# Optimization experiments

Hardware: AMD Instinct MI355X
Metric: run time of the kernel (lower is better)

The kernel has to match this reference:

```python
import jax, jax.numpy as jnp
import numpy as np

N_NODES = 10000
N_EDGES = 320000
IN_DIM = 512
HID = 128


def setup_inputs() -> dict:
    key = jax.random.key(0)
    k1, k2, k3, k4 = jax.random.split(key, 4)
    x = jax.random.normal(k1, (N_NODES, IN_DIM), dtype=jnp.float32)
    edge_index = jax.random.randint(k2, (2, N_EDGES), 0, N_NODES, dtype=jnp.int64)
    W_enc = jax.random.normal(k3, (IN_DIM, HID), dtype=jnp.float32) * 0.05
    b_enc = jnp.zeros((HID,), dtype=jnp.float32)
    W_dec = jax.random.normal(k4, (HID, N_NODES), dtype=jnp.float32) * 0.05
    b_dec = jnp.zeros((N_NODES,), dtype=jnp.float32)
    return {"x": x, "edge_index": edge_index, "W_enc": W_enc, "b_enc": b_enc,
            "W_dec": W_dec, "b_dec": b_dec}


def reference(x, edge_index, W_enc, b_enc, W_dec, b_dec):
    N = x.shape[0]
    # ---- GCNConv (PyG defaults: self-loops + symmetric normalization) ----
    h = x @ W_enc                                  # [N, HID]
    loops = jnp.arange(N, dtype=edge_index.dtype)
    src = jnp.concatenate([edge_index[0], loops])  # source j
    dst = jnp.concatenate([edge_index[1], loops])  # target i
    ones = jnp.ones(src.shape[0], dtype=h.dtype)
    deg = jax.ops.segment_sum(ones, dst, num_segments=N)          # in-degree incl. self-loop
    dinv = jnp.where(deg > 0, jax.lax.rsqrt(deg), 0.0)
    norm = dinv[src] * dinv[dst]                                   # [E+N]
    msgs = h[src] * norm[:, None]                                  # gather-scale
    agg = jax.ops.segment_sum(msgs, dst, num_segments=N)           # scatter-add [N, HID]
    encoded = agg + b_enc
    # ---- decoder: Linear + sigmoid ----
    decoded = jax.nn.sigmoid(encoded @ W_dec + b_dec)              # [N, N]
    return decoded
```

## Files before the change

kernel.cpp:

```cpp
#include <hip/hip_runtime.h>
#include <hip/hip_bf16.h>

#define N_NODES 10000
#define IN_DIM 512
#define HID 128
#define NPAD 10240

typedef __attribute__((ext_vector_type(8))) __bf16 bf16x8;
typedef __attribute__((ext_vector_type(8))) unsigned short u16x8;
typedef __attribute__((ext_vector_type(4))) float f32x4;

__device__ __forceinline__ unsigned short f2bf(float f) {
    unsigned int u = __float_as_uint(f);
    return (unsigned short)((u + 0x7fffu + ((u >> 16) & 1u)) >> 16);
}

__device__ __forceinline__ void gload_lds16(const void* g, void* l) {
    __builtin_amdgcn_global_load_lds(
        (const __attribute__((address_space(1))) unsigned int*)g,
        (__attribute__((address_space(3))) unsigned int*)l, 16, 0, 0);
}

__global__ void k_prep(const float* __restrict__ w, __hip_bfloat16* __restrict__ wT,
                       int* __restrict__ cnt) {
    int b = blockIdx.x;
    if (b < 40) {
        cnt[b * 256 + threadIdx.x] = 0;
        return;
    }
    int idx = (b - 40) * 256 + threadIdx.x;
    int n = idx & (HID - 1);
    int k = idx >> 7;
    wT[n * IN_DIM + k] = __float2bfloat16(w[k * HID + n]);
}

__global__ void k_hist(const int* __restrict__ ei, int* cnt, int E) {
    int e = blockIdx.x * 256 + threadIdx.x;
    if (e < E) atomicAdd(&cnt[ei[E + e]], 1);
}

__global__ __launch_bounds__(1024) void k_scan(
    const int* __restrict__ cnt, int* __restrict__ base,
    int* __restrict__ cursor, float* __restrict__ dinv) {
    __shared__ int lds[1024];
    int t = threadIdx.x;
    int loc[10];
    int sum = 0;
#pragma unroll
    for (int j = 0; j < 10; ++j) {
        int idx = t * 10 + j;
        int c = cnt[idx];
        loc[j] = sum;
        sum += c;
    }
    lds[t] = sum;
    __syncthreads();
    for (int off = 1; off < 1024; off <<= 1) {
        int v = (t >= off) ? lds[t - off] : 0;
        __syncthreads();
        lds[t] += v;
        __syncthreads();
    }
    int ex = lds[t] - sum;
#pragma unroll
    for (int j = 0; j < 10; ++j) {
        int idx = t * 10 + j;
        int b = ex + loc[j];
        base[idx] = b;
        cursor[idx] = b;
        dinv[idx] = rsqrtf((float)cnt[idx] + 1.0f);
    }
}

__global__ void k_fill(const int* __restrict__ ei, const float* __restrict__ dinv,
                       int* cursor, int2* __restrict__ csr, int E) {
    int e = blockIdx.x * 256 + threadIdx.x;
    if (e >= E) return;
    int s = ei[e];
    int d = ei[E + e];
    int pos = atomicAdd(&cursor[d], 1);
    float w = dinv[s] * dinv[d];
    csr[pos] = make_int2(s, __float_as_int(w));
}

__global__ __launch_bounds__(256) void k_wdec_t(const float* __restrict__ wdec,
                                                __hip_bfloat16* __restrict__ wT) {
    __shared__ float tile[32][33];
    int tx = threadIdx.x, ty = threadIdx.y;
    int n0 = blockIdx.x * 32, k0 = blockIdx.y * 32;
#pragma unroll
    for (int j = 0; j < 4; ++j) {
        int k = k0 + ty * 4 + j;
        int n = n0 + tx;
        tile[ty * 4 + j][tx] = (n < N_NODES) ? wdec[(size_t)k * N_NODES + n] : 0.0f;
    }
    __syncthreads();
#pragma unroll
    for (int j = 0; j < 4; ++j) {
        int n = n0 + ty * 4 + j;
        int k = k0 + tx;
        wT[(size_t)n * HID + k] = __float2bfloat16(tile[tx][ty * 4 + j]);
    }
}

__global__ __launch_bounds__(256) void k_enc_gemm(
    const float* __restrict__ x, const __hip_bfloat16* __restrict__ wencT,
    float* __restrict__ h)
{
    int tid = threadIdx.x;
    int wv = tid >> 6, lane = tid & 63;
    int l16 = lane & 15, quad = lane >> 4;
    int m_w = blockIdx.x * 32 + (wv >> 1) * 16;
    int n_w = (wv & 1) * 64;
    f32x4 acc[4] = {};
    int row = m_w + l16;
    bool rv = row < N_NODES;
    const float* xr = x + (size_t)row * IN_DIM;
    for (int kk = 0; kk < IN_DIM; kk += 32) {
        int k0 = kk + quad * 8;
        f32x4 u = {}, w = {};
        if (rv) {
            u = *(const f32x4*)(xr + k0);
            w = *(const f32x4*)(xr + k0 + 4);
        }
        union { u16x8 u; bf16x8 v; } a;
#pragma unroll
        for (int j = 0; j < 4; ++j) {
            a.u[j] = f2bf(u[j]);
            a.u[4 + j] = f2bf(w[j]);
        }
        bf16x8 b[4];
#pragma unroll
        for (int ni = 0; ni < 4; ++ni)
            b[ni] = *(const bf16x8*)(const void*)(wencT + (size_t)(n_w + ni * 16 + l16) * IN_DIM + k0);
#pragma unroll
        for (int ni = 0; ni < 4; ++ni)
            acc[ni] = __builtin_amdgcn_mfma_f32_16x16x32_bf16(a.v, b[ni], acc[ni], 0, 0, 0);
    }
#pragma unroll
    for (int ni = 0; ni < 4; ++ni) {
        int n = n_w + ni * 16 + l16;
#pragma unroll
        for (int r = 0; r < 4; ++r) {
            int m = m_w + quad * 4 + r;
            if (m < N_NODES) h[(size_t)m * HID + n] = acc[ni][r];
        }
    }
}

__global__ __launch_bounds__(256) void k_agg_enc(
    const float* __restrict__ h, const int2* __restrict__ csr,
    const int* __restrict__ base, const int* __restrict__ cnt,
    const float* __restrict__ dinv, const float* __restrict__ b_enc,
    __hip_bfloat16* __restrict__ enc)
{
    int i = blockIdx.x * 2 + (threadIdx.x >> 7);
    int ch = threadIdx.x & 127;
    if (i >= N_NODES) {
        enc[(size_t)i * HID + ch] = __float2bfloat16(0.0f);
        return;
    }
    int lane = threadIdx.x & 63;
    float di = dinv[i];
    float a0 = di * di * h[(size_t)i * HID + ch];
    float a1 = 0.0f, a2 = 0.0f, a3 = 0.0f;
    int j0 = base[i], d = cnt[i];
    for (int b = 0; b < d; b += 64) {
        int cw = d - b;
        if (cw > 64) cw = 64;
        int2 p = make_int2(0, 0);
        if (lane < cw) p = csr[j0 + b + lane];
        int px = p.x, py = p.y;
        int j = 0;
        for (; j + 4 <= cw; j += 4) {
            int s0 = __shfl(px, j),     s1 = __shfl(px, j + 1);
            int s2 = __shfl(px, j + 2), s3 = __shfl(px, j + 3);
            float w0 = __int_as_float(__shfl(py, j));
            float w1 = __int_as_float(__shfl(py, j + 1));
            float w2 = __int_as_float(__shfl(py, j + 2));
            float w3 = __int_as_float(__shfl(py, j + 3));
            a0 += w0 * h[(size_t)s0 * HID + ch];
            a1 += w1 * h[(size_t)s1 * HID + ch];
            a2 += w2 * h[(size_t)s2 * HID + ch];
            a3 += w3 * h[(size_t)s3 * HID + ch];
        }
        for (; j < cw; ++j) {
            int s = __shfl(px, j);
            float w = __int_as_float(__shfl(py, j));
            a0 += w * h[(size_t)s * HID + ch];
        }
    }
    enc[(size_t)i * HID + ch] = __float2bfloat16(((a0 + a1) + (a2 + a3)) + b_enc[ch]);
}

__global__ __launch_bounds__(256) void k_dec_gemm(
    const __hip_bfloat16* __restrict__ A, const __hip_bfloat16* __restrict__ BT,
    const float* __restrict__ bias, float* __restrict__ C)
{
    extern __shared__ char lds[];
    char* ldsA = lds;
    char* ldsB = lds + 32768;

    const int NT = 80;
    int orig = blockIdx.x;
    int wg = (orig & 7) * 800 + (orig >> 3);
    int bx = wg % NT, by = wg / NT;

    int tid = threadIdx.x;
    int wv = tid >> 6, lane = tid & 63;
    int l16 = lane & 15, quad = lane >> 4;
    int wm = wv >> 1, wn = wv & 1;

    {
        const char* gA = (const char*)A + (size_t)by * 32768;
        const char* gB = (const char*)BT + (size_t)bx * 32768;
        int wb = wv * 1024;
#pragma unroll
        for (int it = 0; it < 8; ++it) {
            int L = wb + it * 4096 + lane * 16;
            int row = L >> 8;
            int src = (row << 8) | ((L & 255) ^ ((row & 7) << 4));
            gload_lds16(gA + src, ldsA + wb + it * 4096);
        }
#pragma unroll
        for (int it = 0; it < 8; ++it) {
            int L = wb + it * 4096 + lane * 16;
            int row = L >> 8;
            int src = (row << 8) | ((L & 255) ^ ((row & 7) << 4));
            gload_lds16(gB + src, ldsB + wb + it * 4096);
        }
    }
    asm volatile("s_waitcnt vmcnt(0)" ::: "memory");
    __syncthreads();

    f32x4 acc[4][4] = {};
    int qb = quad * 16;
#pragma unroll
    for (int ks = 0; ks < 4; ++ks) {
        int kb = ks * 64 + qb;
        bf16x8 a[4], b[4];
#pragma unroll
        for (int ni = 0; ni < 4; ++ni) {
            int r = wn * 64 + ni * 16 + l16;
            b[ni] = *(const bf16x8*)(ldsB + ((r << 8) + (kb ^ ((r & 7) << 4))));
        }
#pragma unroll
        for (int mi = 0; mi < 4; ++mi) {
            int r = wm * 64 + mi * 16 + l16;
            a[mi] = *(const bf16x8*)(ldsA + ((r << 8) + (kb ^ ((r & 7) << 4))));
        }
#pragma unroll
        for (int mi = 0; mi < 4; ++mi)
#pragma unroll
            for (int ni = 0; ni < 4; ++ni)
                acc[mi][ni] = __builtin_amdgcn_mfma_f32_16x16x32_bf16(b[ni], a[mi], acc[mi][ni], 0, 0, 0);
    }

    int m_w = by * 128 + wm * 64;
    int n_w = bx * 128 + wn * 64;
    f32x4 bv[4];
#pragma unroll
    for (int ni = 0; ni < 4; ++ni) {
        int n4 = n_w + ni * 16 + quad * 4;
        bv[ni] = (n4 < N_NODES) ? *(const f32x4*)(bias + n4) : f32x4{};
    }
#pragma unroll
    for (int mi = 0; mi < 4; ++mi) {
        int m = m_w + mi * 16 + l16;
        if (m >= N_NODES) continue;
        size_t rowoff = (size_t)m * N_NODES;
#pragma unroll
        for (int ni = 0; ni < 4; ++ni) {
            int n4 = n_w + ni * 16 + quad * 4;
            if (n4 >= N_NODES) continue;
            f32x4 z = acc[mi][ni];
            f32x4 s;
#pragma unroll
            for (int r = 0; r < 4; ++r) {
                float e = __expf(-(z[r] + bv[ni][r]));
                s[r] = __builtin_amdgcn_rcpf(1.0f + e);
            }
            *(f32x4*)(C + rowoff + n4) = s;
        }
    }
}

extern "C" void kernel_launch(void* const* d_in, const int* in_sizes, int n_in,
                              void* d_out, int out_size, void* d_ws, size_t ws_size,
                              hipStream_t stream) {
    const float* x     = (const float*)d_in[0];
    const int*   ei    = (const int*)d_in[1];
    const float* W_enc = (const float*)d_in[2];
    const float* b_enc = (const float*)d_in[3];
    const float* W_dec = (const float*)d_in[4];
    const float* b_dec = (const float*)d_in[5];
    float* out = (float*)d_out;
    const int E = in_sizes[1] / 2;

    char* p = (char*)d_ws;
    auto carve = [&](size_t bytes) -> char* {
        char* r = p;
        p += (bytes + 255) & ~(size_t)255;
        return r;
    };
    int*   cnt    = (int*)carve((size_t)NPAD * 4);
    int*   base   = (int*)carve((size_t)NPAD * 4);
    int*   cursor = (int*)carve((size_t)NPAD * 4);
    float* dinv   = (float*)carve((size_t)NPAD * 4);
    int2*  csr    = (int2*)carve((size_t)E * 8);
    float* h      = (float*)carve((size_t)N_NODES * HID * 4);
    __hip_bfloat16* wencT = (__hip_bfloat16*)carve((size_t)HID * IN_DIM * 2);
    __hip_bfloat16* encb  = (__hip_bfloat16*)carve((size_t)NPAD * HID * 2);
    __hip_bfloat16* wdecT = (__hip_bfloat16*)carve((size_t)NPAD * HID * 2);

    k_prep<<<dim3(40 + HID * IN_DIM / 256), dim3(256), 0, stream>>>(W_enc, wencT, cnt);
    k_hist<<<dim3((E + 255) / 256), dim3(256), 0, stream>>>(ei, cnt, E);
    k_scan<<<dim3(1), dim3(1024), 0, stream>>>(cnt, base, cursor, dinv);
    k_fill<<<dim3((E + 255) / 256), dim3(256), 0, stream>>>(ei, dinv, cursor, csr, E);

    k_wdec_t<<<dim3(NPAD / 32, HID / 32), dim3(32, 8), 0, stream>>>(W_dec, wdecT);

    k_enc_gemm<<<dim3((N_NODES + 31) / 32), dim3(256), 0, stream>>>(x, wencT, h);

    k_agg_enc<<<dim3(NPAD / 2), dim3(256), 0, stream>>>(h, csr, base, cnt, dinv, b_enc, encb);

    k_dec_gemm<<<dim3(80 * 80), dim3(256), 65536, stream>>>(encb, wdecT, b_dec, out);
}
```

Baseline: 548.0 us.

## Fuse W_dec transpose into prep, vectorize aggregation, use nontemporal output stores

Moves the W_dec transpose into the k_prep kernel, which removes one launch. The aggregation kernel now gives each node one wavefront, and each lane handles two channels through float2 loads and a packed bf16 store, so each block covers four nodes instead of two. The decoder writes its large 400 MB output with nontemporal stores to limit cache pollution. The output write dominates the runtime, so the nontemporal store is probably the main lever. The risk is that nontemporal hints may not help write bandwidth on this hardware.

```diff
diff --git a/kernel.cpp b/kernel.cpp
--- a/kernel.cpp
+++ b/kernel.cpp
@@ -9,6 +9,7 @@
 typedef __attribute__((ext_vector_type(8))) __bf16 bf16x8;
 typedef __attribute__((ext_vector_type(8))) unsigned short u16x8;
 typedef __attribute__((ext_vector_type(4))) float f32x4;
+typedef __attribute__((ext_vector_type(2))) float f32x2;
 
 __device__ __forceinline__ unsigned short f2bf(float f) {
     unsigned int u = __float_as_uint(f);
@@ -21,17 +22,42 @@
         (__attribute__((address_space(3))) unsigned int*)l, 16, 0, 0);
 }
 
-__global__ void k_prep(const float* __restrict__ w, __hip_bfloat16* __restrict__ wT,
-                       int* __restrict__ cnt) {
+__global__ __launch_bounds__(256) void k_prep(
+    const float* __restrict__ wenc, __hip_bfloat16* __restrict__ wencT,
+    const float* __restrict__ wdec, __hip_bfloat16* __restrict__ wdecT,
+    int* __restrict__ cnt)
+{
+    __shared__ float tile[32][33];
     int b = blockIdx.x;
+    int tid = threadIdx.x;
     if (b < 40) {
-        cnt[b * 256 + threadIdx.x] = 0;
+        cnt[b * 256 + tid] = 0;
         return;
     }
-    int idx = (b - 40) * 256 + threadIdx.x;
-    int n = idx & (HID - 1);
-    int k = idx >> 7;
-    wT[n * IN_DIM + k] = __float2bfloat16(w[k * HID + n]);
+    if (b < 296) {
+        int idx = (b - 40) * 256 + tid;
+        int n = idx & (HID - 1);
+        int k = idx >> 7;
+        wencT[n * IN_DIM + k] = __float2bfloat16(wenc[k * HID + n]);
+        return;
+    }
+    int t = b - 296;
+    int nb = t % 320, kb = t / 320;
+    int tx = tid & 31, ty = tid >> 5;
+    int n0 = nb * 32, k0 = kb * 32;
+#pragma unroll
+    for (int j = 0; j < 4; ++j) {
+        int k = k0 + ty * 4 + j;
+        int n = n0 + tx;
+        tile[ty * 4 + j][tx] = (n < N_NODES) ? wdec[(size_t)k * N_NODES + n] : 0.0f;
+    }
+    __syncthreads();
+#pragma unroll
+    for (int j = 0; j < 4; ++j) {
+        int n = n0 + ty * 4 + j;
+        int k = k0 + tx;
+        wdecT[(size_t)n * HID + k] = __float2bfloat16(tile[tx][ty * 4 + j]);
+    }
 }
 
 __global__ void k_hist(const int* __restrict__ ei, int* cnt, int E) {
@@ -81,26 +107,6 @@
     int pos = atomicAdd(&cursor[d], 1);
     float w = dinv[s] * dinv[d];
     csr[pos] = make_int2(s, __float_as_int(w));
-}
-
-__global__ __launch_bounds__(256) void k_wdec_t(const float* __restrict__ wdec,
-                                                __hip_bfloat16* __restrict__ wT) {
-    __shared__ float tile[32][33];
-    int tx = threadIdx.x, ty = threadIdx.y;
-    int n0 = blockIdx.x * 32, k0 = blockIdx.y * 32;
-#pragma unroll
-    for (int j = 0; j < 4; ++j) {
-        int k = k0 + ty * 4 + j;
-        int n = n0 + tx;
-        tile[ty * 4 + j][tx] = (n < N_NODES) ? wdec[(size_t)k * N_NODES + n] : 0.0f;
-    }
-    __syncthreads();
-#pragma unroll
-    for (int j = 0; j < 4; ++j) {
-        int n = n0 + ty * 4 + j;
-        int k = k0 + tx;
-        wT[(size_t)n * HID + k] = __float2bfloat16(tile[tx][ty * 4 + j]);
-    }
 }
 
 __global__ __launch_bounds__(256) void k_enc_gemm(
@@ -154,16 +160,17 @@
     const float* __restrict__ dinv, const float* __restrict__ b_enc,
     __hip_bfloat16* __restrict__ enc)
 {
-    int i = blockIdx.x * 2 + (threadIdx.x >> 7);
-    int ch = threadIdx.x & 127;
+    int wv = threadIdx.x >> 6, lane = threadIdx.x & 63;
+    int i = blockIdx.x * 4 + wv;
+    unsigned int* encu = (unsigned int*)enc;
     if (i >= N_NODES) {
-        enc[(size_t)i * HID + ch] = __float2bfloat16(0.0f);
+        encu[(size_t)i * 64 + lane] = 0u;
         return;
     }
-    int lane = threadIdx.x & 63;
+    const f32x2* h2 = (const f32x2*)h;
     float di = dinv[i];
-    float a0 = di * di * h[(size_t)i * HID + ch];
-    float a1 = 0.0f, a2 = 0.0f, a3 = 0.0f;
+    f32x2 a0 = (di * di) * h2[(size_t)i * 64 + lane];
+    f32x2 a1 = {}, a2 = {}, a3 = {};
     int j0 = base[i], d = cnt[i];
     for (int b = 0; b < d; b += 64) {
         int cw = d - b;
@@ -179,18 +186,22 @@
             float w1 = __int_as_float(__shfl(py, j + 1));
             float w2 = __int_as_float(__shfl(py, j + 2));
             float w3 = __int_as_float(__shfl(py, j + 3));
-            a0 += w0 * h[(size_t)s0 * HID + ch];
-            a1 += w1 * h[(size_t)s1 * HID + ch];
-            a2 += w2 * h[(size_t)s2 * HID + ch];
-            a3 += w3 * h[(size_t)s3 * HID + ch];
+            a0 += w0 * h2[(size_t)s0 * 64 + lane];
+            a1 += w1 * h2[(size_t)s1 * 64 + lane];
+            a2 += w2 * h2[(size_t)s2 * 64 + lane];
+            a3 += w3 * h2[(size_t)s3 * 64 + lane];
         }
         for (; j < cw; ++j) {
             int s = __shfl(px, j);
             float w = __int_as_float(__shfl(py, j));
-            a0 += w * h[(size_t)s * HID + ch];
-        }
-    }
-    enc[(size_t)i * HID + ch] = __float2bfloat16(((a0 + a1) + (a2 + a3)) + b_enc[ch]);
+            a0 += w * h2[(size_t)s * 64 + lane];
+        }
+    }
+    f32x2 r = (a0 + a1) + (a2 + a3);
+    f32x2 bb = *(const f32x2*)(b_enc + 2 * lane);
+    r += bb;
+    unsigned int packed = ((unsigned int)f2bf(r[1]) << 16) | (unsigned int)f2bf(r[0]);
+    encu[(size_t)i * 64 + lane] = packed;
 }
 
 __global__ __launch_bounds__(256) void k_dec_gemm(
@@ -280,7 +291,7 @@
                 float e = __expf(-(z[r] + bv[ni][r]));
                 s[r] = __builtin_amdgcn_rcpf(1.0f + e);
             }
-            *(f32x4*)(C + rowoff + n4) = s;
+            __builtin_nontemporal_store(s, (f32x4*)(C + rowoff + n4));
         }
     }
 }
@@ -313,16 +324,14 @@
     __hip_bfloat16* encb  = (__hip_bfloat16*)carve((size_t)NPAD * HID * 2);
     __hip_bfloat16* wdecT = (__hip_bfloat16*)carve((size_t)NPAD * HID * 2);
 
-    k_prep<<<dim3(40 + HID * IN_DIM / 256), dim3(256), 0, stream>>>(W_enc, wencT, cnt);
+    k_prep<<<dim3(40 + 256 + 1280), dim3(256), 0, stream>>>(W_enc, wencT, W_dec, wdecT, cnt);
     k_hist<<<dim3((E + 255) / 256), dim3(256), 0, stream>>>(ei, cnt, E);
     k_scan<<<dim3(1), dim3(1024), 0, stream>>>(cnt, base, cursor, dinv);
     k_fill<<<dim3((E + 255) / 256), dim3(256), 0, stream>>>(ei, dinv, cursor, csr, E);
 
-    k_wdec_t<<<dim3(NPAD / 32, HID / 32), dim3(32, 8), 0, stream>>>(W_dec, wdecT);
-
     k_enc_gemm<<<dim3((N_NODES + 31) / 32), dim3(256), 0, stream>>>(x, wencT, h);
 
-    k_agg_enc<<<dim3(NPAD / 2), dim3(256), 0, stream>>>(h, csr, base, cnt, dinv, b_enc, encb);
+    k_agg_enc<<<dim3(NPAD / 4), dim3(256), 0, stream>>>(h, csr, base, cnt, dinv, b_enc, encb);
 
     k_dec_gemm<<<dim3(80 * 80), dim3(256), 65536, stream>>>(encb, wdecT, b_dec, out);
 }
```

After: 555.0 us. About the same (+1.3%).
